# Optimization experiments

Hardware: AMD Instinct MI355X
Metric: run time of the kernel (lower is better)

Reference implementation:

```python
import jax, jax.numpy as jnp
import numpy as np

HIDDEN = 128
ATT_DIM = 64
ATT_HOPS = 8
B, T, N = 64, 64, 64


def setup_inputs() -> dict:
    key = jax.random.key(0)
    k = jax.random.split(key, 7)
    node = jax.random.normal(k[0], (B, T, HIDDEN), dtype=jnp.float32)
    neigh = jax.random.normal(k[1], (B, N, T * HIDDEN), dtype=jnp.float32)
    neighbors_number = jax.random.randint(k[2], (B,), 1, 64, dtype=jnp.int64 if jax.config.jax_enable_x64 else jnp.int32)
    # nn.Linear params (torch layout: W [out, in])
    s = 1.0 / np.sqrt(HIDDEN)
    W1 = jax.random.uniform(k[3], (ATT_DIM, HIDDEN), jnp.float32, -s, s)
    b1 = jax.random.uniform(k[4], (ATT_DIM,), jnp.float32, -s, s)
    s2 = 1.0 / np.sqrt(ATT_DIM)
    W2 = jax.random.uniform(k[5], (ATT_HOPS, ATT_DIM), jnp.float32, -s2, s2)
    b2 = jax.random.uniform(k[6], (ATT_HOPS,), jnp.float32, -s2, s2)
    return {"node_rnn_output": node, "neigh_rnn_output": neigh,
            "neighbors_number": neighbors_number,
            "W1": W1, "b1": b1, "W2": W2, "b2": b2}


def reference(node_rnn_output, neigh_rnn_output, neighbors_number, W1, b1, W2, b2):
    Bb, Tt, D = node_rnn_output.shape
    Nn = neigh_rnn_output.shape[1]
    L = Nn * Tt
    neigh = neigh_rnn_output.reshape(Bb, L, D)            # [B, N*T, D]
    node_stacked = jnp.tile(node_rnn_output, (1, Nn, 1))  # [B, N*T, D]
    H = neigh * node_stacked                              # elementwise mul
    scale = jnp.sqrt(neighbors_number[0].astype(H.dtype))
    s1 = (jnp.einsum('bld,ad->bla', H, W1) + b1) / scale  # [B, L, att_dim]
    s2 = jnp.einsum('bla,ha->blh', jnp.tanh(s1), W2) + b2 # [B, L, hops]
    A = jax.nn.softmax(jnp.swapaxes(s2, 1, 2), axis=-1)   # [B, hops, L]
    BW = A.sum(axis=1).reshape(Bb, Nn, Tt)                # [B, N, T]
    AAT = jnp.einsum('bhl,bgl->bhg', A, A)                # [B, hops, hops]
    I = jnp.eye(A.shape[1], dtype=A.dtype)
    penal = jnp.sum((AAT - I) ** 2).reshape(1)            # sum of squared Frobenius norms
    return (BW, A, neigh, penal)
```

## Files before the change

kernel.cpp:

```cpp
#include <hip/hip_runtime.h>
#include <hip/hip_bf16.h>
#include <math.h>

#define HID 128
#define ATT 64
#define HOPS 8
#define T_ 64
#define N_ 64
#define B_ 64
#define L_ 4096

typedef __attribute__((ext_vector_type(8))) short bf16x8;
typedef __attribute__((ext_vector_type(4))) float f32x4;

static constexpr size_t OFF_A     = (size_t)B_ * N_ * T_;
static constexpr size_t OFF_NEIGH = OFF_A + (size_t)B_ * HOPS * L_;
static constexpr size_t OFF_PENAL = OFF_NEIGH + (size_t)B_ * L_ * HID;

__device__ __forceinline__ unsigned pkbf(float lo, float hi) {
    unsigned a = (unsigned)(unsigned short)__builtin_bit_cast(unsigned short, __float2bfloat16(lo));
    unsigned b = (unsigned)(unsigned short)__builtin_bit_cast(unsigned short, __float2bfloat16(hi));
    return a | (b << 16);
}
__device__ __forceinline__ short f2bf(float x) {
    return __builtin_bit_cast(short, __float2bfloat16(x));
}

__global__ __launch_bounds__(256, 3)
void k1_mfma(const float* __restrict__ node, const float* __restrict__ neigh,
             const int* __restrict__ nnum, const float* __restrict__ W1,
             const float* __restrict__ b1, const float* __restrict__ W2,
             const float* __restrict__ b2, float* __restrict__ out)
{
    __shared__ unsigned w1lds[64 * 68];
    __shared__ short    thlds[4][16 * 72];

    const int tid  = threadIdx.x;
    const int w    = tid >> 6;
    const int lane = tid & 63;
    const int c    = lane & 15;
    const int g    = lane >> 4;

    const int b  = blockIdx.x >> 4;
    const int l0 = (blockIdx.x & 15) << 8;

    const float* nd = node + ((size_t)b * T_ + (w * 16 + c)) * HID;
    const size_t rowbase = ((size_t)b * L_ + l0 + w * 16 + c) * HID;
    const float* np = neigh + rowbase;
    float*       cp = out + OFF_NEIGH + rowbase;
    float*       s2base = out + OFF_A + (size_t)b * HOPS * L_;

    float4 n[8], abuf[8];
    #pragma unroll
    for (int ks = 0; ks < 4; ++ks) {
        n[2*ks]      = *(const float4*)(nd + ks*32 + g*8);
        n[2*ks+1]    = *(const float4*)(nd + ks*32 + g*8 + 4);
        abuf[2*ks]   = *(const float4*)(np + ks*32 + g*8);
        abuf[2*ks+1] = *(const float4*)(np + ks*32 + g*8 + 4);
    }

    {
        const int a = tid >> 2, q = tid & 3;
        const float* src = W1 + a * HID + q * 32;
        float x[32];
        #pragma unroll
        for (int i = 0; i < 8; ++i) *(float4*)&x[i*4] = *(const float4*)(src + i*4);
        unsigned* dst = &w1lds[a * 68 + q * 16];
        #pragma unroll
        for (int i = 0; i < 16; ++i) dst[i] = pkbf(x[2*i], x[2*i+1]);
    }
    __syncthreads();

    const float inv_scale = rsqrtf((float)nnum[0]);

    bf16x8 wf2[2];
    #pragma unroll
    for (int ks2 = 0; ks2 < 2; ++ks2) {
        union { bf16x8 v; unsigned u[4]; } t;
        #pragma unroll
        for (int i = 0; i < 4; ++i) {
            float lo = (c < 8) ? W2[c*64 + ks2*32 + g*8 + 2*i]     : 0.f;
            float hi = (c < 8) ? W2[c*64 + ks2*32 + g*8 + 2*i + 1] : 0.f;
            t.u[i] = pkbf(lo, hi);
        }
        wf2[ks2] = t.v;
    }
    float b1v[4];
    #pragma unroll
    for (int cf = 0; cf < 4; ++cf) b1v[cf] = b1[cf*16 + c];
    const float b2v = (c < 8) ? b2[c] : 0.f;

    const bf16x8* wptr = reinterpret_cast<const bf16x8*>(&w1lds[c * 68 + g * 4]);
    short* thw = thlds[w];

    #pragma unroll
    for (int it = 0; it < 4; ++it) {
        const int rb = l0 + it * 64 + w * 16;
        float* cpi = cp + (size_t)it * 64 * HID;

        bf16x8 af[4];
        #pragma unroll
        for (int ks = 0; ks < 4; ++ks) {
            *(float4*)(cpi + ks*32 + g*8)     = abuf[2*ks];
            *(float4*)(cpi + ks*32 + g*8 + 4) = abuf[2*ks+1];
            const float4 a0 = abuf[2*ks], a1 = abuf[2*ks+1];
            const float4 n0 = n[2*ks],    n1 = n[2*ks+1];
            union { bf16x8 v; unsigned u[4]; } t;
            t.u[0] = pkbf(a0.x*n0.x, a0.y*n0.y);
            t.u[1] = pkbf(a0.z*n0.z, a0.w*n0.w);
            t.u[2] = pkbf(a1.x*n1.x, a1.y*n1.y);
            t.u[3] = pkbf(a1.z*n1.z, a1.w*n1.w);
            af[ks] = t.v;
        }
        if (it < 3) {
            const float* nx = np + (size_t)(it+1) * 64 * HID;
            #pragma unroll
            for (int ks = 0; ks < 4; ++ks) {
                abuf[2*ks]   = *(const float4*)(nx + ks*32 + g*8);
                abuf[2*ks+1] = *(const float4*)(nx + ks*32 + g*8 + 4);
            }
        }
        f32x4 acc[4];
        #pragma unroll
        for (int cf = 0; cf < 4; ++cf) acc[cf] = (f32x4){0.f,0.f,0.f,0.f};
        #pragma unroll
        for (int cf = 0; cf < 4; ++cf) {
            #pragma unroll
            for (int ks = 0; ks < 4; ++ks)
                acc[cf] = __builtin_amdgcn_mfma_f32_16x16x32_bf16(af[ks], wptr[cf*272 + ks*4], acc[cf], 0, 0, 0);
        }
        #pragma unroll
        for (int cf = 0; cf < 4; ++cf) {
            #pragma unroll
            for (int j = 0; j < 4; ++j) {
                float th = (acc[cf][j] + b1v[cf]) * inv_scale;
                th = 1.0f - 2.0f / (__expf(2.0f * th) + 1.0f);
                thw[(g*4+j)*72 + cf*16 + c] = f2bf(th);
            }
        }
        f32x4 acc2 = (f32x4){0.f,0.f,0.f,0.f};
        #pragma unroll
        for (int ks2 = 0; ks2 < 2; ++ks2) {
            bf16x8 pa = *reinterpret_cast<const bf16x8*>(&thw[c*72 + ks2*32 + g*8]);
            acc2 = __builtin_amdgcn_mfma_f32_16x16x32_bf16(pa, wf2[ks2], acc2, 0, 0, 0);
        }
        if (c < 8) {
            #pragma unroll
            for (int j = 0; j < 4; ++j)
                s2base[(size_t)c * L_ + rb + g*4 + j] = acc2[j] + b2v;
        }
    }
}

__device__ __forceinline__ float waveMax(float v) {
    #pragma unroll
    for (int o = 32; o > 0; o >>= 1) v = fmaxf(v, __shfl_xor(v, o));
    return v;
}
__device__ __forceinline__ float waveSum(float v) {
    #pragma unroll
    for (int o = 32; o > 0; o >>= 1) v += __shfl_xor(v, o);
    return v;
}

__global__ __launch_bounds__(256)
void k2_stats(const float* __restrict__ out, float* __restrict__ stats, float* __restrict__ aat)
{
    const int bh = blockIdx.x;
    const int tid = threadIdx.x;
    if (bh == 0) {
        for (int i = tid; i < B_ * 36; i += 256) aat[i] = 0.f;
    }
    const float* row = out + OFF_A + (size_t)bh * L_;
    __shared__ float red[8];
    float m = -3.4e38f;
    for (int i = tid; i < L_; i += 256) m = fmaxf(m, row[i]);
    m = waveMax(m);
    if ((tid & 63) == 0) red[tid >> 6] = m;
    __syncthreads();
    const float M = fmaxf(fmaxf(red[0], red[1]), fmaxf(red[2], red[3]));
    float s = 0.0f;
    for (int i = tid; i < L_; i += 256) s += __expf(row[i] - M);
    s = waveSum(s);
    if ((tid & 63) == 0) red[4 + (tid >> 6)] = s;
    __syncthreads();
    if (tid == 0) {
        stats[bh * 2]     = M;
        stats[bh * 2 + 1] = red[4] + red[5] + red[6] + red[7];
    }
}

__global__ __launch_bounds__(256)
void k3_soft(float* __restrict__ out, const float* __restrict__ stats, float* __restrict__ aat)
{
    const int blk = blockIdx.x;
    const int b   = blk >> 2;
    const int l0  = (blk & 3) << 10;
    const int tid = threadIdx.x;
    float* A0 = out + OFF_A + (size_t)b * HOPS * L_;
    float* BW = out + (size_t)b * L_;
    float M[HOPS], R[HOPS];
    #pragma unroll
    for (int hh = 0; hh < HOPS; ++hh) {
        M[hh] = stats[(b * HOPS + hh) * 2];
        R[hh] = 1.0f / stats[(b * HOPS + hh) * 2 + 1];
    }
    float p[36];
    #pragma unroll
    for (int i = 0; i < 36; ++i) p[i] = 0.0f;
    for (int l = l0 + tid; l < l0 + 1024; l += 256) {
        float e[HOPS]; float srow = 0.0f;
        #pragma unroll
        for (int hh = 0; hh < HOPS; ++hh) {
            float v = __expf(A0[hh * L_ + l] - M[hh]) * R[hh];
            e[hh] = v; srow += v;
        }
        #pragma unroll
        for (int hh = 0; hh < HOPS; ++hh) A0[hh * L_ + l] = e[hh];
        BW[l] = srow;
        int i = 0;
        #pragma unroll
        for (int hh = 0; hh < HOPS; ++hh) {
            #pragma unroll
            for (int gg = hh; gg < HOPS; ++gg) { p[i] = fmaf(e[hh], e[gg], p[i]); ++i; }
        }
    }
    #pragma unroll
    for (int i = 0; i < 36; ++i) p[i] = waveSum(p[i]);
    __shared__ float red[4][36];
    const int wv = tid >> 6, ln = tid & 63;
    if (ln == 0) {
        #pragma unroll
        for (int i = 0; i < 36; ++i) red[wv][i] = p[i];
    }
    __syncthreads();
    if (tid < 36) {
        float s = red[0][tid] + red[1][tid] + red[2][tid] + red[3][tid];
        atomicAdd(&aat[b * 36 + tid], s);
    }
}

__global__ __launch_bounds__(256)
void k4_penal(const float* __restrict__ aat, float* __restrict__ out)
{
    const int tid = threadIdx.x;
    float s = 0.0f;
    for (int i = tid; i < B_ * 36; i += 256) {
        int r = i % 36;
        bool dg = (r == 0) | (r == 8) | (r == 15) | (r == 21) |
                  (r == 26) | (r == 30) | (r == 33) | (r == 35);
        float d = aat[i] - (dg ? 1.0f : 0.0f);
        float q = d * d;
        s += dg ? q : 2.0f * q;
    }
    s = waveSum(s);
    __shared__ float red[4];
    if ((tid & 63) == 0) red[tid >> 6] = s;
    __syncthreads();
    if (tid == 0) out[OFF_PENAL] = red[0] + red[1] + red[2] + red[3];
}

extern "C" void kernel_launch(void* const* d_in, const int* in_sizes, int n_in,
                              void* d_out, int out_size, void* d_ws, size_t ws_size,
                              hipStream_t stream) {
    const float* node  = (const float*)d_in[0];
    const float* neigh = (const float*)d_in[1];
    const int*   nnum  = (const int*)d_in[2];
    const float* W1    = (const float*)d_in[3];
    const float* b1    = (const float*)d_in[4];
    const float* W2    = (const float*)d_in[5];
    const float* b2    = (const float*)d_in[6];
    float* out   = (float*)d_out;
    float* stats = (float*)d_ws;
    float* aat   = stats + 1024;

    k1_mfma <<<B_ * 16, 256, 0, stream>>>(node, neigh, nnum, W1, b1, W2, b2, out);
    k2_stats<<<B_ * HOPS, 256, 0, stream>>>(out, stats, aat);
    k3_soft <<<256, 256, 0, stream>>>(out, stats, aat);
    k4_penal<<<1, 256, 0, stream>>>(aat, out);
}
```

Measured before the change: 101.5 us.

## Stage coalesced neigh tile through LDS with one 64-row tile per block

The first kernel now handles 64 rows per block (4096 blocks) instead of 256 rows in a 4-iteration register-prefetch loop. Each thread loads fully coalesced contiguous float4s of the neigh tile, writes the copy output, and stores the bf16 elementwise product into an LDS buffer that the MFMA waves then read as A fragments. The aim is to replace the strided per-lane row accesses with contiguous coalesced global traffic and to expose more parallelism for latency hiding. In exchange it adds about 17KB of LDS per block, drops the in-loop prefetch, and reloads W1 into LDS four times as often across the grid.

```diff
diff --git a/kernel.cpp b/kernel.cpp
--- a/kernel.cpp
+++ b/kernel.cpp
@@ -32,123 +32,110 @@
              const float* __restrict__ b1, const float* __restrict__ W2,
              const float* __restrict__ b2, float* __restrict__ out)
 {
-    __shared__ unsigned w1lds[64 * 68];
-    __shared__ short    thlds[4][16 * 72];
+    __shared__ __align__(16) unsigned w1lds[64 * 68];
+    __shared__ __align__(16) unsigned hlds [64 * 68];
+    __shared__ __align__(16) short    thlds[4][16 * 72];
 
     const int tid  = threadIdx.x;
+    const int b    = blockIdx.x >> 6;
+    const int tile = blockIdx.x & 63;
+
+    const size_t base = ((size_t)b * L_ + (size_t)tile * 64) * HID;
+    const float* nb  = neigh + base;
+    float*       cb  = out + OFF_NEIGH + base;
+    const float* ndb = node + (size_t)b * T_ * HID;
+    float*       s2base = out + OFF_A + (size_t)b * HOPS * L_;
+
+    float4 v[8], nv[8];
+    #pragma unroll
+    for (int r = 0; r < 8; ++r)
+        v[r] = *(const float4*)(nb + r * 1024 + tid * 4);
+    const int arow0 = tid >> 5;
+    const int acol  = (tid * 4) & 127;
+    #pragma unroll
+    for (int r = 0; r < 8; ++r)
+        nv[r] = *(const float4*)(ndb + (r * 8 + arow0) * HID + acol);
+    #pragma unroll
+    for (int r = 0; r < 8; ++r) {
+        *(float4*)(cb + r * 1024 + tid * 4) = v[r];
+        const int row = r * 8 + arow0;
+        unsigned p0 = pkbf(v[r].x * nv[r].x, v[r].y * nv[r].y);
+        unsigned p1 = pkbf(v[r].z * nv[r].z, v[r].w * nv[r].w);
+        uint2 pp; pp.x = p0; pp.y = p1;
+        *(uint2*)&hlds[row * 68 + (acol >> 1)] = pp;
+    }
+    {
+        const int a = tid >> 2, q = tid & 3;
+        const float* src = W1 + a * HID + q * 32;
+        float x[32];
+        #pragma unroll
+        for (int i = 0; i < 8; ++i) *(float4*)&x[i * 4] = *(const float4*)(src + i * 4);
+        unsigned* dst = &w1lds[a * 68 + q * 16];
+        #pragma unroll
+        for (int i = 0; i < 16; ++i) dst[i] = pkbf(x[2 * i], x[2 * i + 1]);
+    }
+
     const int w    = tid >> 6;
     const int lane = tid & 63;
     const int c    = lane & 15;
     const int g    = lane >> 4;
-
-    const int b  = blockIdx.x >> 4;
-    const int l0 = (blockIdx.x & 15) << 8;
-
-    const float* nd = node + ((size_t)b * T_ + (w * 16 + c)) * HID;
-    const size_t rowbase = ((size_t)b * L_ + l0 + w * 16 + c) * HID;
-    const float* np = neigh + rowbase;
-    float*       cp = out + OFF_NEIGH + rowbase;
-    float*       s2base = out + OFF_A + (size_t)b * HOPS * L_;
-
-    float4 n[8], abuf[8];
-    #pragma unroll
-    for (int ks = 0; ks < 4; ++ks) {
-        n[2*ks]      = *(const float4*)(nd + ks*32 + g*8);
-        n[2*ks+1]    = *(const float4*)(nd + ks*32 + g*8 + 4);
-        abuf[2*ks]   = *(const float4*)(np + ks*32 + g*8);
-        abuf[2*ks+1] = *(const float4*)(np + ks*32 + g*8 + 4);
-    }
-
-    {
-        const int a = tid >> 2, q = tid & 3;
-        const float* src = W1 + a * HID + q * 32;
-        float x[32];
-        #pragma unroll
-        for (int i = 0; i < 8; ++i) *(float4*)&x[i*4] = *(const float4*)(src + i*4);
-        unsigned* dst = &w1lds[a * 68 + q * 16];
-        #pragma unroll
-        for (int i = 0; i < 16; ++i) dst[i] = pkbf(x[2*i], x[2*i+1]);
-    }
-    __syncthreads();
-
     const float inv_scale = rsqrtf((float)nnum[0]);
 
     bf16x8 wf2[2];
     #pragma unroll
     for (int ks2 = 0; ks2 < 2; ++ks2) {
-        union { bf16x8 v; unsigned u[4]; } t;
+        union { bf16x8 vv; unsigned u[4]; } t;
         #pragma unroll
         for (int i = 0; i < 4; ++i) {
-            float lo = (c < 8) ? W2[c*64 + ks2*32 + g*8 + 2*i]     : 0.f;
-            float hi = (c < 8) ? W2[c*64 + ks2*32 + g*8 + 2*i + 1] : 0.f;
+            float lo = (c < 8) ? W2[c * 64 + ks2 * 32 + g * 8 + 2 * i]     : 0.f;
+            float hi = (c < 8) ? W2[c * 64 + ks2 * 32 + g * 8 + 2 * i + 1] : 0.f;
             t.u[i] = pkbf(lo, hi);
         }
-        wf2[ks2] = t.v;
+        wf2[ks2] = t.vv;
     }
     float b1v[4];
     #pragma unroll
-    for (int cf = 0; cf < 4; ++cf) b1v[cf] = b1[cf*16 + c];
+    for (int cf = 0; cf < 4; ++cf) b1v[cf] = b1[cf * 16 + c];
     const float b2v = (c < 8) ? b2[c] : 0.f;
 
+    __syncthreads();
+
     const bf16x8* wptr = reinterpret_cast<const bf16x8*>(&w1lds[c * 68 + g * 4]);
+    const bf16x8* hptr = reinterpret_cast<const bf16x8*>(&hlds[(w * 16 + c) * 68 + g * 4]);
     short* thw = thlds[w];
 
-    #pragma unroll
-    for (int it = 0; it < 4; ++it) {
-        const int rb = l0 + it * 64 + w * 16;
-        float* cpi = cp + (size_t)it * 64 * HID;
-
-        bf16x8 af[4];
-        #pragma unroll
-        for (int ks = 0; ks < 4; ++ks) {
-            *(float4*)(cpi + ks*32 + g*8)     = abuf[2*ks];
-            *(float4*)(cpi + ks*32 + g*8 + 4) = abuf[2*ks+1];
-            const float4 a0 = abuf[2*ks], a1 = abuf[2*ks+1];
-            const float4 n0 = n[2*ks],    n1 = n[2*ks+1];
-            union { bf16x8 v; unsigned u[4]; } t;
-            t.u[0] = pkbf(a0.x*n0.x, a0.y*n0.y);
-            t.u[1] = pkbf(a0.z*n0.z, a0.w*n0.w);
-            t.u[2] = pkbf(a1.x*n1.x, a1.y*n1.y);
-            t.u[3] = pkbf(a1.z*n1.z, a1.w*n1.w);
-            af[ks] = t.v;
-        }
-        if (it < 3) {
-            const float* nx = np + (size_t)(it+1) * 64 * HID;
-            #pragma unroll
-            for (int ks = 0; ks < 4; ++ks) {
-                abuf[2*ks]   = *(const float4*)(nx + ks*32 + g*8);
-                abuf[2*ks+1] = *(const float4*)(nx + ks*32 + g*8 + 4);
-            }
-        }
-        f32x4 acc[4];
-        #pragma unroll
-        for (int cf = 0; cf < 4; ++cf) acc[cf] = (f32x4){0.f,0.f,0.f,0.f};
-        #pragma unroll
-        for (int cf = 0; cf < 4; ++cf) {
-            #pragma unroll
-            for (int ks = 0; ks < 4; ++ks)
-                acc[cf] = __builtin_amdgcn_mfma_f32_16x16x32_bf16(af[ks], wptr[cf*272 + ks*4], acc[cf], 0, 0, 0);
-        }
-        #pragma unroll
-        for (int cf = 0; cf < 4; ++cf) {
-            #pragma unroll
-            for (int j = 0; j < 4; ++j) {
-                float th = (acc[cf][j] + b1v[cf]) * inv_scale;
-                th = 1.0f - 2.0f / (__expf(2.0f * th) + 1.0f);
-                thw[(g*4+j)*72 + cf*16 + c] = f2bf(th);
-            }
-        }
-        f32x4 acc2 = (f32x4){0.f,0.f,0.f,0.f};
-        #pragma unroll
-        for (int ks2 = 0; ks2 < 2; ++ks2) {
-            bf16x8 pa = *reinterpret_cast<const bf16x8*>(&thw[c*72 + ks2*32 + g*8]);
-            acc2 = __builtin_amdgcn_mfma_f32_16x16x32_bf16(pa, wf2[ks2], acc2, 0, 0, 0);
-        }
-        if (c < 8) {
-            #pragma unroll
-            for (int j = 0; j < 4; ++j)
-                s2base[(size_t)c * L_ + rb + g*4 + j] = acc2[j] + b2v;
-        }
+    bf16x8 af[4];
+    #pragma unroll
+    for (int ks = 0; ks < 4; ++ks) af[ks] = hptr[ks * 4];
+
+    f32x4 acc[4];
+    #pragma unroll
+    for (int cf = 0; cf < 4; ++cf) acc[cf] = (f32x4){0.f, 0.f, 0.f, 0.f};
+    #pragma unroll
+    for (int cf = 0; cf < 4; ++cf) {
+        #pragma unroll
+        for (int ks = 0; ks < 4; ++ks)
+            acc[cf] = __builtin_amdgcn_mfma_f32_16x16x32_bf16(af[ks], wptr[cf * 272 + ks * 4], acc[cf], 0, 0, 0);
+    }
+    #pragma unroll
+    for (int cf = 0; cf < 4; ++cf) {
+        #pragma unroll
+        for (int j = 0; j < 4; ++j) {
+            float th = (acc[cf][j] + b1v[cf]) * inv_scale;
+            th = 1.0f - 2.0f / (__expf(2.0f * th) + 1.0f);
+            thw[(g * 4 + j) * 72 + cf * 16 + c] = f2bf(th);
+        }
+    }
+    f32x4 acc2 = (f32x4){0.f, 0.f, 0.f, 0.f};
+    #pragma unroll
+    for (int ks2 = 0; ks2 < 2; ++ks2) {
+        bf16x8 pa = *reinterpret_cast<const bf16x8*>(&thw[c * 72 + ks2 * 32 + g * 8]);
+        acc2 = __builtin_amdgcn_mfma_f32_16x16x32_bf16(pa, wf2[ks2], acc2, 0, 0, 0);
+    }
+    if (c < 8) {
+        const int rb = tile * 64 + w * 16;
+        float4 o; o.x = acc2[0] + b2v; o.y = acc2[1] + b2v; o.z = acc2[2] + b2v; o.w = acc2[3] + b2v;
+        *(float4*)&s2base[(size_t)c * L_ + rb + g * 4] = o;
     }
 }
 
@@ -274,7 +261,7 @@
     float* stats = (float*)d_ws;
     float* aat   = stats + 1024;
 
-    k1_mfma <<<B_ * 16, 256, 0, stream>>>(node, neigh, nnum, W1, b1, W2, b2, out);
+    k1_mfma <<<B_ * 64, 256, 0, stream>>>(node, neigh, nnum, W1, b1, W2, b2, out);
     k2_stats<<<B_ * HOPS, 256, 0, stream>>>(out, stats, aat);
     k3_soft <<<256, 256, 0, stream>>>(out, stats, aat);
     k4_penal<<<1, 256, 0, stream>>>(aat, out);
```

Result: slower. 105.5 us (+3.9%).
